# Kernel tuning notes

Measured on AMD Instinct MI355X. Metric: run time of the kernel, lower is better.

The kernel has to match this reference:

```python
import jax, jax.numpy as jnp
import numpy as np

N_TOKENS = 8192
EMBED = 1024
HIDDEN = 4 * EMBED
NUM_EXPERTS = 8


def setup_inputs() -> dict:
    key = jax.random.key(0)
    ks = jax.random.split(key, 10)
    s = 0.02
    return {
        "x": jax.random.normal(ks[0], (N_TOKENS, EMBED), dtype=jnp.float32),
        # Router params
        "Wr1": jax.random.normal(ks[1], (EMBED, EMBED), dtype=jnp.float32) * s,
        "br1": jnp.zeros((EMBED,), dtype=jnp.float32),
        "Wr2": jax.random.normal(ks[2], (EMBED, NUM_EXPERTS), dtype=jnp.float32) * s,
        "br2": jnp.zeros((NUM_EXPERTS,), dtype=jnp.float32),
        # Expert FFN params, stacked over experts
        "W1": jax.random.normal(ks[3], (NUM_EXPERTS, EMBED, HIDDEN), dtype=jnp.float32) * s,
        "b1": jnp.zeros((NUM_EXPERTS, HIDDEN), dtype=jnp.float32),
        "W2": jax.random.normal(ks[4], (NUM_EXPERTS, HIDDEN, EMBED), dtype=jnp.float32) * s,
        "b2": jnp.zeros((NUM_EXPERTS, EMBED), dtype=jnp.float32),
    }


def reference(x, Wr1, br1, Wr2, br2, W1, b1, W2, b2):
    # Router: Linear -> ReLU -> Linear -> softmax over experts -> top-1
    h = jax.nn.relu(x @ Wr1 + br1)                      # [N, E]
    probs = jax.nn.softmax(h @ Wr2 + br2, axis=1)       # [N, num_experts]
    chosen = jnp.argmax(probs, axis=1)                  # [N]

    num_experts = W1.shape[0]
    out = jnp.zeros_like(x)
    # Fixed small loop over experts (structurally distinct weights).
    for e in range(num_experts):
        ffn_e = jax.nn.relu(x @ W1[e] + b1[e]) @ W2[e] + b2[e]  # [N, E]
        out = jnp.where((chosen == e)[:, None], ffn_e, out)
    # Note: original returns raw expert output (no probability weighting).
    return out
```

## Files before the change

kernel.cpp:

```cpp
#include <hip/hip_runtime.h>
#include <stdint.h>

#define N_TOK 8192
#define EMB 1024
#define HID 4096
#define NEXP 8

typedef _Float16 f16x8 __attribute__((ext_vector_type(8)));
typedef _Float16 f16x4 __attribute__((ext_vector_type(4)));
typedef short    s16x8 __attribute__((ext_vector_type(8)));
typedef unsigned short u16x8 __attribute__((ext_vector_type(8)));
typedef float    f32x4 __attribute__((ext_vector_type(4)));

typedef __attribute__((address_space(1))) const void gvoid_t;
typedef __attribute__((address_space(3))) void lvoid_t;

__device__ __forceinline__ void async16(const void* g, void* l) {
  __builtin_amdgcn_global_load_lds((gvoid_t*)g, (lvoid_t*)l, 16, 0, 0);
}

__device__ __forceinline__ unsigned short f2bf(float f) {
  unsigned u = __builtin_bit_cast(unsigned, f);
  u += 0x7fffu + ((u >> 16) & 1u);
  return (unsigned short)(u >> 16);
}

__global__ __launch_bounds__(256) void k_cast_x(const float* __restrict__ x,
    unsigned short* __restrict__ xb, _Float16* __restrict__ xhi, _Float16* __restrict__ xlo) {
  int i = (blockIdx.x * 256 + threadIdx.x) << 2;
  float4 v = *(const float4*)(x + i);
  ushort4 b;
  b.x = f2bf(v.x); b.y = f2bf(v.y); b.z = f2bf(v.z); b.w = f2bf(v.w);
  *(ushort4*)(xb + i) = b;
  float vv[4] = {v.x, v.y, v.z, v.w};
  f16x4 hi, lo;
#pragma unroll
  for (int j = 0; j < 4; j++) {
    _Float16 h = (_Float16)vv[j];
    hi[j] = h;
    lo[j] = (_Float16)(vv[j] - (float)h);
  }
  *(f16x4*)(xhi + i) = hi;
  *(f16x4*)(xlo + i) = lo;
}

__global__ __launch_bounds__(256) void k_trans_wr1(const float* __restrict__ src,
    _Float16* __restrict__ dhi, _Float16* __restrict__ dlo) {
  int nblk = blockIdx.x >> 4, kc = blockIdx.x & 15;
  int n = (nblk << 8) + threadIdx.x;
  int k0 = kc << 6;
  for (int k = k0; k < k0 + 64; k += 8) {
    f16x8 hi, lo;
#pragma unroll
    for (int j = 0; j < 8; j++) {
      float w = src[(size_t)(k + j) * EMB + n] * 256.0f;
      _Float16 h = (_Float16)w;
      hi[j] = h;
      lo[j] = (_Float16)(w - (float)h);
    }
    *(f16x8*)(dhi + (size_t)n * EMB + k) = hi;
    *(f16x8*)(dlo + (size_t)n * EMB + k) = lo;
  }
}

__global__ __launch_bounds__(256) void k_transcast_v2(const float* __restrict__ src,
    unsigned short* __restrict__ dst, int K, int Nn, int ktiles, int ntiles) {
  __shared__ __align__(16) unsigned short lds[256 * 72];
  int b = blockIdx.x;
  int e = b / (ktiles * ntiles);
  int r = b % (ktiles * ntiles);
  int kt = r / ntiles, nt = r % ntiles;
  int k0 = kt << 6, n0 = nt << 8;
  const float* s = src + (size_t)e * K * Nn;
  unsigned short* d = dst + (size_t)e * K * Nn;
  int tid = threadIdx.x;
  const float* scol = s + n0 + tid;
#pragma unroll 4
  for (int k = 0; k < 64; k += 2) {
    float a  = scol[(size_t)(k0 + k) * Nn];
    float bv = scol[(size_t)(k0 + k + 1) * Nn];
    unsigned p = (unsigned)f2bf(a) | ((unsigned)f2bf(bv) << 16);
    *(unsigned*)(lds + tid * 72 + k) = p;
  }
  __syncthreads();
  int c = tid & 7, nl = tid >> 3;
#pragma unroll
  for (int p2 = 0; p2 < 8; p2++) {
    int n = (p2 << 5) + nl;
    u16x8 v = *(const u16x8*)(lds + n * 72 + (c << 3));
    *(u16x8*)(d + (size_t)(n0 + n) * K + k0 + (c << 3)) = v;
  }
}

__global__ __launch_bounds__(256) void k_router_gemm(
    const _Float16* __restrict__ Ah, const _Float16* __restrict__ Al,
    const _Float16* __restrict__ Bh, const _Float16* __restrict__ Bl,
    const float* __restrict__ br1, float* __restrict__ hOut) {
  __shared__ __align__(16) _Float16 sAh[4096], sAl[4096], sBh[4096], sBl[4096];
  const int tid = threadIdx.x, lane = tid & 63, wave = tid >> 6;
  const int m0 = (blockIdx.x >> 3) << 7;
  const int n0 = (blockIdx.x & 7) << 7;
  const int srow = (wave << 5) + (lane >> 2);
  const int scol = (lane & 3) << 3;
  const size_t aBase = (size_t)(m0 + srow) * EMB + scol;
  const size_t bBase = (size_t)(n0 + srow) * EMB + scol;
  _Float16* lAh = sAh + (wave << 10);
  _Float16* lAl = sAl + (wave << 10);
  _Float16* lBh = sBh + (wave << 10);
  _Float16* lBl = sBl + (wave << 10);
  const int q = lane >> 4, c = lane & 15;
  const int msub = (wave & 1) << 6, nsub = (wave >> 1) << 6;
  f32x4 acc[4][4];
#pragma unroll
  for (int i = 0; i < 4; i++)
#pragma unroll
    for (int j = 0; j < 4; j++) acc[i][j] = (f32x4){0.f, 0.f, 0.f, 0.f};

  for (int kk = 0; kk < EMB; kk += 32) {
    async16(Ah + aBase + kk, lAh);
    async16(Ah + aBase + 16 * EMB + kk, lAh + 512);
    async16(Al + aBase + kk, lAl);
    async16(Al + aBase + 16 * EMB + kk, lAl + 512);
    async16(Bh + bBase + kk, lBh);
    async16(Bh + bBase + 16 * EMB + kk, lBh + 512);
    async16(Bl + bBase + kk, lBl);
    async16(Bl + bBase + 16 * EMB + kk, lBl + 512);
    __syncthreads();
    f16x8 fah[4], fal[4], fbh[4], fbl[4];
#pragma unroll
    for (int i = 0; i < 4; i++) {
      int ar = msub + (i << 4) + c;
      int br = nsub + (i << 4) + c;
      fah[i] = *(const f16x8*)(sAh + (ar << 5) + (q << 3));
      fal[i] = *(const f16x8*)(sAl + (ar << 5) + (q << 3));
      fbh[i] = *(const f16x8*)(sBh + (br << 5) + (q << 3));
      fbl[i] = *(const f16x8*)(sBl + (br << 5) + (q << 3));
    }
#pragma unroll
    for (int mi = 0; mi < 4; mi++)
#pragma unroll
      for (int ni = 0; ni < 4; ni++) {
        acc[mi][ni] = __builtin_amdgcn_mfma_f32_16x16x32_f16(fah[mi], fbh[ni], acc[mi][ni], 0, 0, 0);
        acc[mi][ni] = __builtin_amdgcn_mfma_f32_16x16x32_f16(fah[mi], fbl[ni], acc[mi][ni], 0, 0, 0);
        acc[mi][ni] = __builtin_amdgcn_mfma_f32_16x16x32_f16(fal[mi], fbh[ni], acc[mi][ni], 0, 0, 0);
      }
    __syncthreads();
  }
#pragma unroll
  for (int mi = 0; mi < 4; mi++)
#pragma unroll
    for (int ni = 0; ni < 4; ni++) {
      int gn = n0 + nsub + (ni << 4) + c;
      float bias = 256.0f * br1[gn];
#pragma unroll
      for (int i2 = 0; i2 < 4; i2++) {
        int gm = m0 + msub + (mi << 4) + (q << 2) + i2;
        float v = acc[mi][ni][i2] + bias;
        hOut[(size_t)gm * EMB + gn] = v > 0.f ? v : 0.f;
      }
    }
}

__global__ __launch_bounds__(256) void k_logits(const float* __restrict__ h,
    const float* __restrict__ Wr2, const float* __restrict__ br2, int* __restrict__ chosen) {
  __shared__ __align__(16) float sW[EMB * NEXP];
  int tid = threadIdx.x;
  for (int i = tid; i < EMB * NEXP; i += 256) sW[i] = Wr2[i];
  __syncthreads();
  int lane = tid & 63, wave = tid >> 6;
  int t = blockIdx.x * 4 + wave;
  const float* hr = h + (size_t)t * EMB;
  float acc[8] = {0.f, 0.f, 0.f, 0.f, 0.f, 0.f, 0.f, 0.f};
#pragma unroll
  for (int i = 0; i < 16; i++) {
    int k = (i << 6) + lane;
    float v = hr[k];
    float4 w0 = *(const float4*)(sW + (k << 3));
    float4 w1 = *(const float4*)(sW + (k << 3) + 4);
    acc[0] += v * w0.x; acc[1] += v * w0.y; acc[2] += v * w0.z; acc[3] += v * w0.w;
    acc[4] += v * w1.x; acc[5] += v * w1.y; acc[6] += v * w1.z; acc[7] += v * w1.w;
  }
#pragma unroll
  for (int off = 32; off > 0; off >>= 1)
#pragma unroll
    for (int e = 0; e < 8; e++) acc[e] += __shfl_down(acc[e], off);
  if (lane == 0) {
    float best = acc[0] + 256.0f * br2[0];
    int bi = 0;
#pragma unroll
    for (int e = 1; e < 8; e++) {
      float l = acc[e] + 256.0f * br2[e];
      if (l > best) { best = l; bi = e; }
    }
    chosen[t] = bi;
  }
}

__global__ void k_zero(int* meta) { meta[threadIdx.x] = 0; }

__global__ __launch_bounds__(256) void k_hist(const int* __restrict__ chosen, int* meta) {
  int i = blockIdx.x * 256 + threadIdx.x;
  atomicAdd(&meta[chosen[i]], 1);
}

__global__ __launch_bounds__(128) void k_sched(int* meta) {
  __shared__ int cnt[8];
  int tid = threadIdx.x;
  if (tid < 8) cnt[tid] = meta[tid];
  __syncthreads();
  int off[9]; off[0] = 0;
#pragma unroll
  for (int e = 0; e < 8; e++) off[e + 1] = off[e] + cnt[e];
  int ts[9]; ts[0] = 0;
#pragma unroll
  for (int e = 0; e < 8; e++) ts[e + 1] = ts[e] + ((cnt[e] + 127) >> 7);
  int T = ts[8];
  if (tid < 8) meta[16 + tid] = off[tid];
  if (tid == 0) { meta[24] = off[8]; meta[25] = T; }
  if (tid < T) {
    int e = 0;
    while (ts[e + 1] <= tid) e++;
    int m = off[e] + ((tid - ts[e]) << 7);
    int end = off[e + 1];
    meta[32 + tid] = e;
    meta[112 + tid] = m;
    meta[192 + tid] = (m + 128 < end) ? m + 128 : end;
  }
}

__global__ __launch_bounds__(256) void k_scatter(const int* __restrict__ chosen,
                                                 int* meta, int* __restrict__ perm) {
  int i = blockIdx.x * 256 + threadIdx.x;
  int e = chosen[i];
  int pos = meta[16 + e] + atomicAdd(&meta[8 + e], 1);
  perm[pos] = i;
}

__global__ __launch_bounds__(256) void k_ffn1(
    const unsigned short* __restrict__ xb, const unsigned short* __restrict__ w1t,
    const float* __restrict__ b1, const int* __restrict__ perm,
    const int* __restrict__ meta, unsigned short* __restrict__ hidden) {
  const int mt = blockIdx.x >> 5;
  if (mt >= meta[25]) return;
  const int nt = blockIdx.x & 31;
  const int e = meta[32 + mt];
  const int row0 = meta[112 + mt];
  const int rend = meta[192 + mt];
  const int n0 = nt << 7;
  __shared__ __align__(16) unsigned short sA[4096], sB[4096];
  const int tid = threadIdx.x, lane = tid & 63, wave = tid >> 6;
  const int srow = (wave << 5) + (lane >> 2);
  const int scol = (lane & 3) << 3;
  int ra0 = row0 + srow, ra1 = row0 + srow + 16;
  if (ra0 > rend - 1) ra0 = rend - 1;
  if (ra1 > rend - 1) ra1 = rend - 1;
  const int t0 = perm[ra0], t1 = perm[ra1];
  const unsigned short* a0 = xb + (size_t)t0 * EMB + scol;
  const unsigned short* a1 = xb + (size_t)t1 * EMB + scol;
  const unsigned short* bsrc = w1t + (size_t)e * EMB * HID + (size_t)(n0 + srow) * EMB + scol;
  unsigned short* lA = sA + (wave << 10);
  unsigned short* lB = sB + (wave << 10);
  const int q = lane >> 4, c = lane & 15;
  const int msub = (wave & 1) << 6, nsub = (wave >> 1) << 6;
  f32x4 acc[4][4];
#pragma unroll
  for (int i = 0; i < 4; i++)
#pragma unroll
    for (int j = 0; j < 4; j++) acc[i][j] = (f32x4){0.f, 0.f, 0.f, 0.f};

  for (int kk = 0; kk < EMB; kk += 32) {
    async16(a0 + kk, lA);
    async16(a1 + kk, lA + 512);
    async16(bsrc + kk, lB);
    async16(bsrc + 16 * EMB + kk, lB + 512);
    __syncthreads();
    s16x8 fa[4], fb[4];
#pragma unroll
    for (int i = 0; i < 4; i++) {
      fa[i] = *(const s16x8*)(sA + ((msub + (i << 4) + c) << 5) + (q << 3));
      fb[i] = *(const s16x8*)(sB + ((nsub + (i << 4) + c) << 5) + (q << 3));
    }
#pragma unroll
    for (int mi = 0; mi < 4; mi++)
#pragma unroll
      for (int ni = 0; ni < 4; ni++)
        acc[mi][ni] = __builtin_amdgcn_mfma_f32_16x16x32_bf16(fa[mi], fb[ni], acc[mi][ni], 0, 0, 0);
    __syncthreads();
  }
#pragma unroll
  for (int mi = 0; mi < 4; mi++)
#pragma unroll
    for (int ni = 0; ni < 4; ni++) {
      int gn = n0 + nsub + (ni << 4) + c;
      float bias = b1[e * HID + gn];
#pragma unroll
      for (int i2 = 0; i2 < 4; i2++) {
        int rs = row0 + msub + (mi << 4) + (q << 2) + i2;
        if (rs < rend) {
          float v = acc[mi][ni][i2] + bias;
          v = v > 0.f ? v : 0.f;
          hidden[(size_t)rs * HID + gn] = f2bf(v);
        }
      }
    }
}

__global__ __launch_bounds__(256) void k_ffn2(
    const unsigned short* __restrict__ hidden, const unsigned short* __restrict__ w2t,
    const float* __restrict__ b2, const int* __restrict__ perm,
    const int* __restrict__ meta, float* __restrict__ out) {
  const int mt = blockIdx.x >> 3;
  if (mt >= meta[25]) return;
  const int nt = blockIdx.x & 7;
  const int e = meta[32 + mt];
  const int row0 = meta[112 + mt];
  const int rend = meta[192 + mt];
  const int n0 = nt << 7;
  __shared__ __align__(16) unsigned short sA[4096], sB[4096];
  const int tid = threadIdx.x, lane = tid & 63, wave = tid >> 6;
  const int srow = (wave << 5) + (lane >> 2);
  const int scol = (lane & 3) << 3;
  int ra0 = row0 + srow, ra1 = row0 + srow + 16;
  if (ra0 > N_TOK - 1) ra0 = N_TOK - 1;
  if (ra1 > N_TOK - 1) ra1 = N_TOK - 1;
  const unsigned short* a0 = hidden + (size_t)ra0 * HID + scol;
  const unsigned short* a1 = hidden + (size_t)ra1 * HID + scol;
  const unsigned short* bsrc = w2t + (size_t)e * HID * EMB + (size_t)(n0 + srow) * HID + scol;
  unsigned short* lA = sA + (wave << 10);
  unsigned short* lB = sB + (wave << 10);
  const int q = lane >> 4, c = lane & 15;
  const int msub = (wave & 1) << 6, nsub = (wave >> 1) << 6;
  f32x4 acc[4][4];
#pragma unroll
  for (int i = 0; i < 4; i++)
#pragma unroll
    for (int j = 0; j < 4; j++) acc[i][j] = (f32x4){0.f, 0.f, 0.f, 0.f};

  for (int kk = 0; kk < HID; kk += 32) {
    async16(a0 + kk, lA);
    async16(a1 + kk, lA + 512);
    async16(bsrc + kk, lB);
    async16(bsrc + 16 * HID + kk, lB + 512);
    __syncthreads();
    s16x8 fa[4], fb[4];
#pragma unroll
    for (int i = 0; i < 4; i++) {
      fa[i] = *(const s16x8*)(sA + ((msub + (i << 4) + c) << 5) + (q << 3));
      fb[i] = *(const s16x8*)(sB + ((nsub + (i << 4) + c) << 5) + (q << 3));
    }
#pragma unroll
    for (int mi = 0; mi < 4; mi++)
#pragma unroll
      for (int ni = 0; ni < 4; ni++)
        acc[mi][ni] = __builtin_amdgcn_mfma_f32_16x16x32_bf16(fa[mi], fb[ni], acc[mi][ni], 0, 0, 0);
    __syncthreads();
  }
#pragma unroll
  for (int mi = 0; mi < 4; mi++)
#pragma unroll
    for (int ni = 0; ni < 4; ni++) {
      int gn = n0 + nsub + (ni << 4) + c;
      float bias = b2[e * EMB + gn];
#pragma unroll
      for (int i2 = 0; i2 < 4; i2++) {
        int rs = row0 + msub + (mi << 4) + (q << 2) + i2;
        if (rs < rend) {
          int orig = perm[rs];
          out[(size_t)orig * EMB + gn] = acc[mi][ni][i2] + bias;
        }
      }
    }
}

extern "C" void kernel_launch(void* const* d_in, const int* in_sizes, int n_in,
                              void* d_out, int out_size, void* d_ws, size_t ws_size,
                              hipStream_t stream) {
  const float* x   = (const float*)d_in[0];
  const float* Wr1 = (const float*)d_in[1];
  const float* br1 = (const float*)d_in[2];
  const float* Wr2 = (const float*)d_in[3];
  const float* br2 = (const float*)d_in[4];
  const float* W1  = (const float*)d_in[5];
  const float* b1  = (const float*)d_in[6];
  const float* W2  = (const float*)d_in[7];
  const float* b2  = (const float*)d_in[8];
  float* out = (float*)d_out;
  char* ws = (char*)d_ws;

  unsigned short* w1t    = (unsigned short*)(ws + 0);
  unsigned short* w2t    = (unsigned short*)(ws + 67108864);
  unsigned short* xb     = (unsigned short*)(ws + 134217728);
  _Float16*       xhi    = (_Float16*)(ws + 150994944);
  _Float16*       xlo    = (_Float16*)(ws + 167772160);
  _Float16*       whi    = (_Float16*)(ws + 184549376);
  _Float16*       wlo    = (_Float16*)(ws + 186646528);
  float*          hbuf   = (float*)(ws + 188743680);
  unsigned short* hidden = (unsigned short*)(ws + 222298112);
  int*            chosen = (int*)(ws + 289406976);
  int*            perm   = (int*)(ws + 289439744);
  int*            meta   = (int*)(ws + 289472512);

  k_cast_x<<<dim3(8192), dim3(256), 0, stream>>>(x, xb, xhi, xlo);
  k_trans_wr1<<<dim3(64), dim3(256), 0, stream>>>(Wr1, whi, wlo);
  k_transcast_v2<<<dim3(2048), dim3(256), 0, stream>>>(W1, w1t, 1024, 4096, 16, 16);
  k_transcast_v2<<<dim3(2048), dim3(256), 0, stream>>>(W2, w2t, 4096, 1024, 64, 4);
  k_router_gemm<<<dim3(512), dim3(256), 0, stream>>>(xhi, xlo, whi, wlo, br1, hbuf);
  k_logits<<<dim3(2048), dim3(256), 0, stream>>>(hbuf, Wr2, br2, chosen);
  k_zero<<<dim3(1), dim3(256), 0, stream>>>(meta);
  k_hist<<<dim3(32), dim3(256), 0, stream>>>(chosen, meta);
  k_sched<<<dim3(1), dim3(128), 0, stream>>>(meta);
  k_scatter<<<dim3(32), dim3(256), 0, stream>>>(chosen, meta, perm);
  k_ffn1<<<dim3(2304), dim3(256), 0, stream>>>(xb, w1t, b1, perm, meta, hidden);
  k_ffn2<<<dim3(576), dim3(256), 0, stream>>>(hidden, w2t, b2, perm, meta, out);
}
```

Measured before the change: 773.3 us.

## Enlarge expert GEMM tiles to 256 rows with K=64 steps and swizzled LDS

The expert FFN kernels move from 128x128 tiles with 4 waves to 256x128 tiles with 8 waves. A second schedule with 256-row segments per expert is added to the scheduler. Each K step now loads 64 columns into LDS, using an XOR swizzle to avoid bank conflicts, which halves the number of barriers and improves weight reuse per block. The cost is more LDS per block (48KB), fewer blocks, and more padding waste on partial expert segments.

After: 766.3 us. About the same (-0.9%).

```diff
diff --git a/kernel.cpp b/kernel.cpp
--- a/kernel.cpp
+++ b/kernel.cpp
@@ -211,11 +211,11 @@
   int off[9]; off[0] = 0;
 #pragma unroll
   for (int e = 0; e < 8; e++) off[e + 1] = off[e] + cnt[e];
+  if (tid < 8) meta[16 + tid] = off[tid];
   int ts[9]; ts[0] = 0;
 #pragma unroll
   for (int e = 0; e < 8; e++) ts[e + 1] = ts[e] + ((cnt[e] + 127) >> 7);
   int T = ts[8];
-  if (tid < 8) meta[16 + tid] = off[tid];
   if (tid == 0) { meta[24] = off[8]; meta[25] = T; }
   if (tid < T) {
     int e = 0;
@@ -226,6 +226,20 @@
     meta[112 + tid] = m;
     meta[192 + tid] = (m + 128 < end) ? m + 128 : end;
   }
+  int ts2[9]; ts2[0] = 0;
+#pragma unroll
+  for (int e = 0; e < 8; e++) ts2[e + 1] = ts2[e] + ((cnt[e] + 255) >> 8);
+  int T2 = ts2[8];
+  if (tid == 0) meta[26] = T2;
+  if (tid < T2) {
+    int e = 0;
+    while (ts2[e + 1] <= tid) e++;
+    int m = off[e] + ((tid - ts2[e]) << 8);
+    int end = off[e + 1];
+    meta[288 + tid] = e;
+    meta[368 + tid] = m;
+    meta[448 + tid] = (m + 256 < end) ? m + 256 : end;
+  }
 }
 
 __global__ __launch_bounds__(256) void k_scatter(const int* __restrict__ chosen,
@@ -236,55 +250,67 @@
   perm[pos] = i;
 }
 
-__global__ __launch_bounds__(256) void k_ffn1(
+__global__ __launch_bounds__(512) void k_ffn1(
     const unsigned short* __restrict__ xb, const unsigned short* __restrict__ w1t,
     const float* __restrict__ b1, const int* __restrict__ perm,
     const int* __restrict__ meta, unsigned short* __restrict__ hidden) {
   const int mt = blockIdx.x >> 5;
-  if (mt >= meta[25]) return;
+  if (mt >= meta[26]) return;
   const int nt = blockIdx.x & 31;
-  const int e = meta[32 + mt];
-  const int row0 = meta[112 + mt];
-  const int rend = meta[192 + mt];
+  const int e = meta[288 + mt];
+  const int row0 = meta[368 + mt];
+  const int rend = meta[448 + mt];
   const int n0 = nt << 7;
-  __shared__ __align__(16) unsigned short sA[4096], sB[4096];
+  __shared__ __align__(16) unsigned short sA[256 * 64], sB[128 * 64];
   const int tid = threadIdx.x, lane = tid & 63, wave = tid >> 6;
-  const int srow = (wave << 5) + (lane >> 2);
-  const int scol = (lane & 3) << 3;
-  int ra0 = row0 + srow, ra1 = row0 + srow + 16;
-  if (ra0 > rend - 1) ra0 = rend - 1;
-  if (ra1 > rend - 1) ra1 = rend - 1;
-  const int t0 = perm[ra0], t1 = perm[ra1];
-  const unsigned short* a0 = xb + (size_t)t0 * EMB + scol;
-  const unsigned short* a1 = xb + (size_t)t1 * EMB + scol;
-  const unsigned short* bsrc = w1t + (size_t)e * EMB * HID + (size_t)(n0 + srow) * EMB + scol;
-  unsigned short* lA = sA + (wave << 10);
-  unsigned short* lB = sB + (wave << 10);
+  const int lr = lane >> 3;
+  const int scol = ((lane & 7) ^ lr) << 3;
+  const unsigned short* aptr[4];
+#pragma unroll
+  for (int j = 0; j < 4; j++) {
+    int r = row0 + (wave << 5) + (j << 3) + lr;
+    if (r > N_TOK - 1) r = N_TOK - 1;
+    aptr[j] = xb + (size_t)perm[r] * EMB + scol;
+  }
+  const unsigned short* bptr[2];
+#pragma unroll
+  for (int j = 0; j < 2; j++) {
+    int r = n0 + (wave << 4) + (j << 3) + lr;
+    bptr[j] = w1t + (size_t)e * EMB * HID + (size_t)r * EMB + scol;
+  }
   const int q = lane >> 4, c = lane & 15;
-  const int msub = (wave & 1) << 6, nsub = (wave >> 1) << 6;
+  const int msub = (wave >> 1) << 6;
+  const int nsub = (wave & 1) << 6;
   f32x4 acc[4][4];
 #pragma unroll
   for (int i = 0; i < 4; i++)
 #pragma unroll
     for (int j = 0; j < 4; j++) acc[i][j] = (f32x4){0.f, 0.f, 0.f, 0.f};
 
-  for (int kk = 0; kk < EMB; kk += 32) {
-    async16(a0 + kk, lA);
-    async16(a1 + kk, lA + 512);
-    async16(bsrc + kk, lB);
-    async16(bsrc + 16 * EMB + kk, lB + 512);
-    __syncthreads();
-    s16x8 fa[4], fb[4];
-#pragma unroll
-    for (int i = 0; i < 4; i++) {
-      fa[i] = *(const s16x8*)(sA + ((msub + (i << 4) + c) << 5) + (q << 3));
-      fb[i] = *(const s16x8*)(sB + ((nsub + (i << 4) + c) << 5) + (q << 3));
-    }
-#pragma unroll
-    for (int mi = 0; mi < 4; mi++)
-#pragma unroll
-      for (int ni = 0; ni < 4; ni++)
-        acc[mi][ni] = __builtin_amdgcn_mfma_f32_16x16x32_bf16(fa[mi], fb[ni], acc[mi][ni], 0, 0, 0);
+#pragma unroll 1
+  for (int kk = 0; kk < EMB; kk += 64) {
+    async16(aptr[0] + kk, sA + ((wave << 5) + 0)  * 64);
+    async16(aptr[1] + kk, sA + ((wave << 5) + 8)  * 64);
+    async16(aptr[2] + kk, sA + ((wave << 5) + 16) * 64);
+    async16(aptr[3] + kk, sA + ((wave << 5) + 24) * 64);
+    async16(bptr[0] + kk, sB + ((wave << 4) + 0)  * 64);
+    async16(bptr[1] + kk, sB + ((wave << 4) + 8)  * 64);
+    __syncthreads();
+#pragma unroll
+    for (int ks = 0; ks < 2; ks++) {
+      const int coff = ((((ks << 2) + q) ^ (c & 7)) << 3);
+      s16x8 fa[4], fb[4];
+#pragma unroll
+      for (int i = 0; i < 4; i++) {
+        fa[i] = *(const s16x8*)(sA + ((msub + (i << 4) + c) << 6) + coff);
+        fb[i] = *(const s16x8*)(sB + ((nsub + (i << 4) + c) << 6) + coff);
+      }
+#pragma unroll
+      for (int mi = 0; mi < 4; mi++)
+#pragma unroll
+        for (int ni = 0; ni < 4; ni++)
+          acc[mi][ni] = __builtin_amdgcn_mfma_f32_16x16x32_bf16(fa[mi], fb[ni], acc[mi][ni], 0, 0, 0);
+    }
     __syncthreads();
   }
 #pragma unroll
@@ -305,54 +331,67 @@
     }
 }
 
-__global__ __launch_bounds__(256) void k_ffn2(
+__global__ __launch_bounds__(512) void k_ffn2(
     const unsigned short* __restrict__ hidden, const unsigned short* __restrict__ w2t,
     const float* __restrict__ b2, const int* __restrict__ perm,
     const int* __restrict__ meta, float* __restrict__ out) {
   const int mt = blockIdx.x >> 3;
-  if (mt >= meta[25]) return;
+  if (mt >= meta[26]) return;
   const int nt = blockIdx.x & 7;
-  const int e = meta[32 + mt];
-  const int row0 = meta[112 + mt];
-  const int rend = meta[192 + mt];
+  const int e = meta[288 + mt];
+  const int row0 = meta[368 + mt];
+  const int rend = meta[448 + mt];
   const int n0 = nt << 7;
-  __shared__ __align__(16) unsigned short sA[4096], sB[4096];
+  __shared__ __align__(16) unsigned short sA[256 * 64], sB[128 * 64];
   const int tid = threadIdx.x, lane = tid & 63, wave = tid >> 6;
-  const int srow = (wave << 5) + (lane >> 2);
-  const int scol = (lane & 3) << 3;
-  int ra0 = row0 + srow, ra1 = row0 + srow + 16;
-  if (ra0 > N_TOK - 1) ra0 = N_TOK - 1;
-  if (ra1 > N_TOK - 1) ra1 = N_TOK - 1;
-  const unsigned short* a0 = hidden + (size_t)ra0 * HID + scol;
-  const unsigned short* a1 = hidden + (size_t)ra1 * HID + scol;
-  const unsigned short* bsrc = w2t + (size_t)e * HID * EMB + (size_t)(n0 + srow) * HID + scol;
-  unsigned short* lA = sA + (wave << 10);
-  unsigned short* lB = sB + (wave << 10);
+  const int lr = lane >> 3;
+  const int scol = ((lane & 7) ^ lr) << 3;
+  const unsigned short* aptr[4];
+#pragma unroll
+  for (int j = 0; j < 4; j++) {
+    int r = row0 + (wave << 5) + (j << 3) + lr;
+    if (r > N_TOK - 1) r = N_TOK - 1;
+    aptr[j] = hidden + (size_t)r * HID + scol;
+  }
+  const unsigned short* bptr[2];
+#pragma unroll
+  for (int j = 0; j < 2; j++) {
+    int r = n0 + (wave << 4) + (j << 3) + lr;
+    bptr[j] = w2t + (size_t)e * HID * EMB + (size_t)r * HID + scol;
+  }
   const int q = lane >> 4, c = lane & 15;
-  const int msub = (wave & 1) << 6, nsub = (wave >> 1) << 6;
+  const int msub = (wave >> 1) << 6;
+  const int nsub = (wave & 1) << 6;
   f32x4 acc[4][4];
 #pragma unroll
   for (int i = 0; i < 4; i++)
 #pragma unroll
     for (int j = 0; j < 4; j++) acc[i][j] = (f32x4){0.f, 0.f, 0.f, 0.f};
 
-  for (int kk = 0; kk < HID; kk += 32) {
-    async16(a0 + kk, lA);
-    async16(a1 + kk, lA + 512);
-    async16(bsrc + kk, lB);
-    async16(bsrc + 16 * HID + kk, lB + 512);
-    __syncthreads();
-    s16x8 fa[4], fb[4];
-#pragma unroll
-    for (int i = 0; i < 4; i++) {
-      fa[i] = *(const s16x8*)(sA + ((msub + (i << 4) + c) << 5) + (q << 3));
-      fb[i] = *(const s16x8*)(sB + ((nsub + (i << 4) + c) << 5) + (q << 3));
-    }
-#pragma unroll
-    for (int mi = 0; mi < 4; mi++)
-#pragma unroll
-      for (int ni = 0; ni < 4; ni++)
-        acc[mi][ni] = __builtin_amdgcn_mfma_f32_16x16x32_bf16(fa[mi], fb[ni], acc[mi][ni], 0, 0, 0);
+#pragma unroll 1
+  for (int kk = 0; kk < HID; kk += 64) {
+    async16(aptr[0] + kk, sA + ((wave << 5) + 0)  * 64);
+    async16(aptr[1] + kk, sA + ((wave << 5) + 8)  * 64);
+    async16(aptr[2] + kk, sA + ((wave << 5) + 16) * 64);
+    async16(aptr[3] + kk, sA + ((wave << 5) + 24) * 64);
+    async16(bptr[0] + kk, sB + ((wave << 4) + 0)  * 64);
+    async16(bptr[1] + kk, sB + ((wave << 4) + 8)  * 64);
+    __syncthreads();
+#pragma unroll
+    for (int ks = 0; ks < 2; ks++) {
+      const int coff = ((((ks << 2) + q) ^ (c & 7)) << 3);
+      s16x8 fa[4], fb[4];
+#pragma unroll
+      for (int i = 0; i < 4; i++) {
+        fa[i] = *(const s16x8*)(sA + ((msub + (i << 4) + c) << 6) + coff);
+        fb[i] = *(const s16x8*)(sB + ((nsub + (i << 4) + c) << 6) + coff);
+      }
+#pragma unroll
+      for (int mi = 0; mi < 4; mi++)
+#pragma unroll
+        for (int ni = 0; ni < 4; ni++)
+          acc[mi][ni] = __builtin_amdgcn_mfma_f32_16x16x32_bf16(fa[mi], fb[ni], acc[mi][ni], 0, 0, 0);
+    }
     __syncthreads();
   }
 #pragma unroll
@@ -410,6 +449,6 @@
   k_hist<<<dim3(32), dim3(256), 0, stream>>>(chosen, meta);
   k_sched<<<dim3(1), dim3(128), 0, stream>>>(meta);
   k_scatter<<<dim3(32), dim3(256), 0, stream>>>(chosen, meta, perm);
-  k_ffn1<<<dim3(2304), dim3(256), 0, stream>>>(xb, w1t, b1, perm, meta, hidden);
-  k_ffn2<<<dim3(576), dim3(256), 0, stream>>>(hidden, w2t, b2, perm, meta, out);
-}
+  k_ffn1<<<dim3(1280), dim3(512), 0, stream>>>(xb, w1t, b1, perm, meta, hidden);
+  k_ffn2<<<dim3(320), dim3(512), 0, stream>>>(hidden, w2t, b2, perm, meta, out);
+}
```
